# Performance work log

Hardware: AMD Instinct MI355X
Metric: run time of the kernel (lower is better)

Reference implementation:

```python
import jax, jax.numpy as jnp
import numpy as np

B, C, H, W = 4, 256, 64, 64
EPS = 1e-5

def conv1x1(x, w, b):
    # x: [B,Cin,H,W], w: [Cout,Cin], b: [Cout]
    return jnp.einsum('bchw,oc->bohw', x, w) + b[None, :, None, None]

def setup_inputs() -> dict:
    key = jax.random.key(0)
    ks = jax.random.split(key, 16)
    s = 1.0 / np.sqrt(C)
    d = {
        'x1': jax.random.normal(ks[0], (B, C, H, W), jnp.float32),
        'x2': jax.random.normal(ks[1], (B, C, H, W), jnp.float32),
        'q_w': jax.random.normal(ks[2], (C, C), jnp.float32) * s,
        'q_b': jnp.zeros((C,), jnp.float32),
        'k_w': jax.random.normal(ks[3], (C, C), jnp.float32) * s,
        'k_b': jnp.zeros((C,), jnp.float32),
        'v_w': jax.random.normal(ks[4], (C, C), jnp.float32) * s,
        'v_b': jnp.zeros((C,), jnp.float32),
        'proj_w': jax.random.normal(ks[5], (C, C), jnp.float32) * s,
        'proj_b': jnp.zeros((C,), jnp.float32),
        'bn_gamma': jnp.ones((C,), jnp.float32),
        'bn_beta': jnp.zeros((C,), jnp.float32),
        'bn_mean': jax.random.normal(ks[6], (C,), jnp.float32) * 0.1,
        'bn_var': jax.random.uniform(ks[7], (C,), jnp.float32, 0.5, 1.5),
        'gate_w': jax.random.normal(ks[8], (1, 2 * C), jnp.float32) * (1.0 / np.sqrt(2 * C)),
        'gate_b': jnp.zeros((1,), jnp.float32),
    }
    return d

def reference(x1, x2, q_w, q_b, k_w, k_b, v_w, v_b, proj_w, proj_b,
              bn_gamma, bn_beta, bn_mean, bn_var, gate_w, gate_b):
    b, c, h, w = x1.shape
    n = h * w
    scale = c ** (-0.5)
    q = conv1x1(x1, q_w, q_b).reshape(b, c, n)   # [B,C,N]
    k = conv1x1(x2, k_w, k_b).reshape(b, c, n)
    v = conv1x1(x2, v_w, v_b).reshape(b, c, n)
    attn = jnp.einsum('bcn,bcm->bnm', q, k) * scale      # [B,N,N]
    attn = jax.nn.softmax(attn, axis=-1)
    fusion = jnp.einsum('bcm,bnm->bcn', v, attn)          # v @ attn^T
    fusion = fusion.reshape(b, c, h, w)
    # proj: conv1x1 -> BN (eval, running stats) -> ReLU
    fusion = conv1x1(fusion, proj_w, proj_b)
    fusion = (fusion - bn_mean[None, :, None, None]) * (
        bn_gamma[None, :, None, None] * jax.lax.rsqrt(bn_var + EPS)[None, :, None, None]
    ) + bn_beta[None, :, None, None]
    fusion = jax.nn.relu(fusion)
    gate = jax.nn.sigmoid(conv1x1(jnp.concatenate([x1, x2], axis=1), gate_w, gate_b))  # [B,1,H,W]
    return x1 + gate * fusion
```

## Files before the change

### kernel.cpp

```cpp
#include <hip/hip_runtime.h>
#include <hip/hip_bf16.h>
#include <hip/hip_fp8.h>

#define NB   4
#define C    256
#define NPIX 4096
#define EPSV 1e-5f
#define K2   0.09016844f
#define MFIX 24.0f
#define KVB  32
#define NSPLIT 4
#define NKVS (NPIX / NSPLIT)
#define NSTEPS (NKVS / KVB)

typedef __bf16 bf16x8 __attribute__((ext_vector_type(8)));
typedef float  f32x4  __attribute__((ext_vector_type(4)));
typedef float  f32x16 __attribute__((ext_vector_type(16)));
typedef unsigned int u32x4 __attribute__((ext_vector_type(4)));
typedef __hip_bfloat16 bf16;

__device__ __forceinline__ void gload16(const void* g, void* l) {
    __builtin_amdgcn_global_load_lds(
        (const __attribute__((address_space(1))) void*)g,
        (__attribute__((address_space(3))) void*)l, 16, 0, 0);
}

__device__ __forceinline__ unsigned char to_fp8(float x) {
    return __hip_fp8_e4m3(x).__x;
}

__global__ __launch_bounds__(256) void k_transpose(
    const float* __restrict__ x1, const float* __restrict__ x2,
    const float* __restrict__ gate_w,
    const float* __restrict__ qw, const float* __restrict__ kw,
    const float* __restrict__ vw, const float* __restrict__ pw,
    bf16* __restrict__ xt1, bf16* __restrict__ xt2,
    float* __restrict__ gate_ws, bf16* __restrict__ wb)
{
    __shared__ float tile[64][65];
    const int t = threadIdx.x;
    const int z = blockIdx.z;

    if (z == 8) {
        const int sub = blockIdx.x * 4 + blockIdx.y;
        const int i0 = sub * 1024 + t * 4;
        bf16 t4[4];
#pragma unroll
        for (int j = 0; j < 4; ++j) {
            const int i = i0 + j;
            const int p = i >> 16, rem = i & 65535;
            const int o = rem >> 8, cp = rem & 255;
            const int c = cp ^ ((o & 7) << 3);
            const float* w = (p == 0) ? qw : (p == 1) ? kw : (p == 2) ? vw : pw;
            t4[j] = __float2bfloat16(w[o * 256 + c]);
        }
        *reinterpret_cast<uint64_t*>(wb + i0) = *reinterpret_cast<uint64_t*>(t4);
        return;
    }

    const int nt = blockIdx.x, ct = blockIdx.y;
    const int b = z >> 1, which = z & 1;
    const float* x = which ? x2 : x1;
    bf16* xt = which ? xt2 : xt1;
    const int n0 = nt * 64, c0 = ct * 64;

    const float* xp = x + ((size_t)b * C + c0) * NPIX + n0;
#pragma unroll
    for (int i = 0; i < 16; ++i) {
        int cl = (t >> 6) + i * 4, nl = t & 63;
        tile[cl][nl] = xp[(size_t)cl * NPIX + nl];
    }
    __syncthreads();

    {
        int nl = t & 63, qq = t >> 6;
        float s = 0.f;
#pragma unroll
        for (int i = 0; i < 16; ++i) {
            int cl = qq * 16 + i;
            s += tile[cl][nl] * gate_w[which * C + c0 + cl];
        }
        atomicAdd(&gate_ws[b * NPIX + n0 + nl], s);
    }

    bf16* xtp = xt + ((size_t)b * NPIX + n0) * C + c0;
#pragma unroll
    for (int i = 0; i < 16; ++i) {
        int nl = (t >> 6) + i * 4, cl = t & 63;
        xtp[(size_t)nl * C + cl] = __float2bfloat16(tile[cl][nl]);
    }
}

__global__ __launch_bounds__(256) void k_qkv(
    const bf16* __restrict__ xt1, const bf16* __restrict__ xt2,
    const bf16* __restrict__ wb,
    const float* __restrict__ qb, const float* __restrict__ kb,
    const float* __restrict__ vb,
    unsigned char* __restrict__ Qt, unsigned char* __restrict__ Kt,
    bf16* __restrict__ Vv)
{
    __shared__ __align__(16) char wl[32768];
    const int nblk = blockIdx.x, ot = blockIdx.y, zp = blockIdx.z;
    const int b = zp / 3, pidx = zp % 3;
    const bf16* xt = (pidx == 0) ? xt1 : xt2;
    const float* bias = (pidx == 0) ? qb : (pidx == 1) ? kb : vb;
    const int o0 = ot * 64;
    const int t = threadIdx.x;
    const int wave = t >> 6, lane = t & 63;
    const int g = lane >> 4, l15 = lane & 15;

    {
        const char* src = (const char*)(wb + ((size_t)pidx * C + o0) * C);
#pragma unroll
        for (int i = 0; i < 8; ++i) {
            const int L = i * 4096 + t * 16;
            gload16(src + L, wl + L);
        }
    }
    asm volatile("s_waitcnt vmcnt(0)" ::: "memory");
    __syncthreads();

    bf16x8 a[4][8];
#pragma unroll
    for (int ns = 0; ns < 4; ++ns) {
        const bf16* xrow = xt + ((size_t)b * NPIX + nblk * 256 + wave * 64 + ns * 16 + l15) * C;
#pragma unroll
        for (int cb = 0; cb < 8; ++cb)
            a[ns][cb] = *reinterpret_cast<const bf16x8*>(xrow + cb * 32 + 8 * g);
    }

#pragma unroll
    for (int os = 0; os < 4; ++os) {
        const int oo = o0 + os * 16;
        bf16x8 wf[8];
#pragma unroll
        for (int cb = 0; cb < 8; ++cb)
            wf[cb] = *reinterpret_cast<const bf16x8*>(
                wl + (os * 16 + l15) * 512 + ((cb * 64 + 16 * g) ^ ((l15 & 7) << 4)));

        f32x4 acc[4] = {{0,0,0,0},{0,0,0,0},{0,0,0,0},{0,0,0,0}};
#pragma unroll
        for (int cb = 0; cb < 8; ++cb) {
#pragma unroll
            for (int ns = 0; ns < 4; ++ns) {
                if (pidx < 2)
                    acc[ns] = __builtin_amdgcn_mfma_f32_16x16x32_bf16(a[ns][cb], wf[cb], acc[ns], 0, 0, 0);
                else
                    acc[ns] = __builtin_amdgcn_mfma_f32_16x16x32_bf16(wf[cb], a[ns][cb], acc[ns], 0, 0, 0);
            }
        }

        if (pidx < 2) {
            const float bv = bias[oo + l15];
            const float scl = (pidx == 0) ? K2 : 1.0f;
            unsigned char* Qk = (pidx == 0) ? Qt : Kt;
#pragma unroll
            for (int ns = 0; ns < 4; ++ns) {
                const int n0 = nblk * 256 + wave * 64 + ns * 16;
                unsigned char* dst = Qk + ((size_t)b * NPIX + n0 + 4 * g) * C + oo + l15;
#pragma unroll
                for (int r = 0; r < 4; ++r)
                    dst[(size_t)r * C] = to_fp8((acc[ns][r] + bv) * scl);
            }
        } else {
#pragma unroll
            for (int ns = 0; ns < 4; ++ns) {
                const int n0 = nblk * 256 + wave * 64 + ns * 16;
                bf16* dst = Vv + ((size_t)b * C + oo + 4 * g) * NPIX + n0 + l15;
#pragma unroll
                for (int r = 0; r < 4; ++r)
                    dst[(size_t)r * NPIX] = __float2bfloat16(acc[ns][r] + bias[oo + 4 * g + r]);
            }
        }
    }
}

#define SMEM_ATTN 49152
#define SZP ((size_t)NPIX * C)

__global__ __launch_bounds__(256, 2) void k_attn(
    const unsigned char* __restrict__ Qt, const unsigned char* __restrict__ Kt,
    const bf16* __restrict__ Vv, bf16* __restrict__ O0,
    bf16* __restrict__ O1, float2* __restrict__ mlws)
{
    extern __shared__ __align__(16) char smem[];
    const int id = blockIdx.x;
    const int combo = id & 15, nt = id >> 4;
    const int b = combo >> 2, split = combo & 3;
    const int m_base = split * NKVS;
    const int tid = threadIdx.x;
    const int wave = tid >> 6, lane = tid & 63;
    const int dl = lane & 31, hi = lane >> 5;
    const int n0 = nt * 128 + wave * 32;

    const unsigned char* Kg = Kt + (size_t)b * NPIX * C;
    const bf16* Vg = Vv + (size_t)b * C * NPIX;

    int o_k[2], o_v[4];
#pragma unroll
    for (int p = 0; p < 2; ++p) {
        const int L = p * 4096 + tid * 16;
        const int kv = L >> 8;
        const int col = (L & 255) ^ ((kv & 15) << 4);
        o_k[p] = kv * C + col;
    }
#pragma unroll
    for (int p = 0; p < 4; ++p) {
        const int L = p * 4096 + tid * 16;
        const int R = L >> 7, colx2 = L & 127;
        const int col2 = colx2 ^ (((L >> 8) & 7) << 4);
        const int d = 2 * R + (col2 >> 6);
        o_v[p] = d * NPIX + ((col2 & 63) >> 1);
    }

    long q[16];
    const unsigned char* qrow = Qt + ((size_t)b * NPIX + n0 + dl) * C + 8 * hi;
#pragma unroll
    for (int cs = 0; cs < 16; ++cs)
        q[cs] = *reinterpret_cast<const long*>(qrow + cs * 16);

    const int kRow = dl * 256, kmask = (dl & 15) << 4;
    const int vRow = (dl >> 1) * 128;
    const int vc0  = (((dl & 1) << 6) | (16 * hi)) ^ (((dl >> 2) & 7) << 4);

    f32x16 o[8];
#pragma unroll
    for (int i = 0; i < 8; ++i)
#pragma unroll
        for (int j = 0; j < 16; ++j) o[i][j] = 0.f;
    float l_run = 0.f;

    auto stage = [&](int buf, int m0) {
        char* kd = smem + buf * 24576;
        char* vd = kd + 8192;
#pragma unroll
        for (int p = 0; p < 2; ++p)
            gload16(Kg + (size_t)m0 * C + o_k[p], kd + p * 4096 + tid * 16);
#pragma unroll
        for (int p = 0; p < 4; ++p)
            gload16(Vg + o_v[p] + m0, vd + p * 4096 + tid * 16);
    };

    stage(0, m_base);
    asm volatile("s_waitcnt vmcnt(0)" ::: "memory");
    __syncthreads();

    for (int t = 0; t < NSTEPS; ++t) {
        const int buf = t & 1;
        if (t + 1 < NSTEPS) stage(buf ^ 1, m_base + (t + 1) * KVB);

        const char* Kl = smem + buf * 24576;
        const char* Vl = Kl + 8192;

        f32x16 s;
#pragma unroll
        for (int j = 0; j < 16; ++j) s[j] = 0.f;
        __builtin_amdgcn_s_setprio(1);
#pragma unroll
        for (int cs = 0; cs < 16; ++cs) {
            long kf = *reinterpret_cast<const long*>(
                Kl + kRow + ((cs * 16 + 8 * hi) ^ kmask));
            s = __builtin_amdgcn_mfma_f32_32x32x16_fp8_fp8(kf, q[cs], s, 0, 0, 0);
        }
        __builtin_amdgcn_s_setprio(0);

        float psum = 0.f;
#pragma unroll
        for (int j = 0; j < 16; ++j) {
            s[j] = exp2f(s[j] - MFIX);
            psum += s[j];
        }
        psum += __shfl_xor(psum, 32);
        l_run += psum;

        unsigned w[8];
#pragma unroll
        for (int i = 0; i < 8; ++i) {
            asm("v_cvt_pk_bf16_f32 %0, %1, %2"
                : "=v"(w[i]) : "v"(s[2 * i]), "v"(s[2 * i + 1]));
        }
        asm("v_permlane32_swap_b32 %0, %1" : "+v"(w[0]), "+v"(w[2]));
        asm("v_permlane32_swap_b32 %0, %1" : "+v"(w[1]), "+v"(w[3]));
        asm("v_permlane32_swap_b32 %0, %1" : "+v"(w[4]), "+v"(w[6]));
        asm("v_permlane32_swap_b32 %0, %1" : "+v"(w[5]), "+v"(w[7]));
        const bf16x8 pb0 = __builtin_bit_cast(bf16x8, (u32x4){w[0], w[1], w[2], w[3]});
        const bf16x8 pb1 = __builtin_bit_cast(bf16x8, (u32x4){w[4], w[5], w[6], w[7]});

        __builtin_amdgcn_s_setprio(1);
#pragma unroll
        for (int dt = 0; dt < 8; ++dt) {
            bf16x8 vf0 = *reinterpret_cast<const bf16x8*>(Vl + dt * 2048 + vRow + vc0);
            o[dt] = __builtin_amdgcn_mfma_f32_32x32x16_bf16(vf0, pb0, o[dt], 0, 0, 0);
            bf16x8 vf1 = *reinterpret_cast<const bf16x8*>(Vl + dt * 2048 + vRow + (vc0 ^ 32));
            o[dt] = __builtin_amdgcn_mfma_f32_32x32x16_bf16(vf1, pb1, o[dt], 0, 0, 0);
        }
        __builtin_amdgcn_s_setprio(0);

        asm volatile("s_waitcnt vmcnt(0)" ::: "memory");
        __syncthreads();
    }

    const int pp = split * NB + b;
    bf16* base = (pp < 8) ? (O0 + (size_t)pp * SZP) : (O1 + (size_t)(pp - 8) * SZP);
    const float invl = 1.0f / l_run;
    bf16* orow = base + (size_t)(n0 + dl) * C;
#pragma unroll
    for (int dt = 0; dt < 8; ++dt) {
#pragma unroll
        for (int a = 0; a < 4; ++a) {
            bf16 t4[4];
#pragma unroll
            for (int r = 0; r < 4; ++r)
                t4[r] = __float2bfloat16(o[dt][4 * a + r] * invl);
            *reinterpret_cast<uint64_t*>(orow + dt * 32 + 8 * a + 4 * hi) =
                *reinterpret_cast<uint64_t*>(t4);
        }
    }
    if (lane < 32)
        mlws[(size_t)pp * NPIX + n0 + dl] = make_float2(MFIX, l_run);
}

__global__ __launch_bounds__(256) void k_combine(
    const bf16* __restrict__ O0, const bf16* __restrict__ O1,
    const float2* __restrict__ ml, bf16* __restrict__ Ot)
{
    const int tid = blockIdx.x * 256 + threadIdx.x;
    const int c8 = tid & 31;
    const int rest = tid >> 5;
    const int n = rest & 4095;
    const int b = rest >> 12;

    float2 a[NSPLIT];
#pragma unroll
    for (int s = 0; s < NSPLIT; ++s)
        a[s] = ml[(size_t)(s * NB + b) * NPIX + n];
    float M = fmaxf(fmaxf(a[0].x, a[1].x), fmaxf(a[2].x, a[3].x));
    float w[NSPLIT], tot = 0.f;
#pragma unroll
    for (int s = 0; s < NSPLIT; ++s) { w[s] = exp2f(a[s].x - M) * a[s].y; tot += w[s]; }
    float rs = 1.0f / tot;
#pragma unroll
    for (int s = 0; s < NSPLIT; ++s) w[s] *= rs;

    const size_t off = (size_t)n * C + c8 * 8;
    float acc[8] = {0,0,0,0,0,0,0,0};
#pragma unroll
    for (int s = 0; s < NSPLIT; ++s) {
        const int pp = s * NB + b;
        const bf16* src = ((pp < 8) ? (O0 + (size_t)pp * SZP)
                                    : (O1 + (size_t)(pp - 8) * SZP)) + off;
        bf16x8 x = *reinterpret_cast<const bf16x8*>(src);
#pragma unroll
        for (int j = 0; j < 8; ++j) acc[j] += w[s] * (float)x[j];
    }
    bf16 outv[8];
#pragma unroll
    for (int j = 0; j < 8; ++j) outv[j] = __float2bfloat16(acc[j]);
    *reinterpret_cast<bf16x8*>(Ot + ((size_t)b * NPIX + n) * C + c8 * 8) =
        *reinterpret_cast<bf16x8*>(outv);
}

__global__ __launch_bounds__(256) void k_proj(
    const bf16* __restrict__ Ot, const bf16* __restrict__ wb,
    const float* __restrict__ pb, const float* __restrict__ bn_g,
    const float* __restrict__ bn_b, const float* __restrict__ bn_m,
    const float* __restrict__ bn_v, const float* __restrict__ gate_ws,
    const float* __restrict__ gate_b, const float* __restrict__ x1,
    float* __restrict__ out)
{
    __shared__ __align__(16) char wl[32768];
    const int nblk = blockIdx.x, ot = blockIdx.y, b = blockIdx.z;
    const int o0 = ot * 64;
    const int t = threadIdx.x;
    const int wave = t >> 6, lane = t & 63;
    const int g = lane >> 4, l15 = lane & 15;

    {
        const char* src = (const char*)(wb + ((size_t)3 * C + o0) * C);
#pragma unroll
        for (int i = 0; i < 8; ++i) {
            const int L = i * 4096 + t * 16;
            gload16(src + L, wl + L);
        }
    }
    asm volatile("s_waitcnt vmcnt(0)" ::: "memory");
    __syncthreads();

    bf16x8 bfr[2][8];
#pragma unroll
    for (int ns = 0; ns < 2; ++ns) {
        const bf16* orow = Ot + ((size_t)b * NPIX + nblk * 128 + wave * 32 + ns * 16 + l15) * C;
#pragma unroll
        for (int cb = 0; cb < 8; ++cb)
            bfr[ns][cb] = *reinterpret_cast<const bf16x8*>(orow + cb * 32 + 8 * g);
    }
    const float gb = gate_b[0];

#pragma unroll
    for (int os = 0; os < 4; ++os) {
        const int oo = o0 + os * 16;
        bf16x8 wf[8];
#pragma unroll
        for (int cb = 0; cb < 8; ++cb)
            wf[cb] = *reinterpret_cast<const bf16x8*>(
                wl + (os * 16 + l15) * 512 + ((cb * 64 + 16 * g) ^ ((l15 & 7) << 4)));

        f32x4 acc[2] = {{0,0,0,0},{0,0,0,0}};
#pragma unroll
        for (int cb = 0; cb < 8; ++cb) {
            acc[0] = __builtin_amdgcn_mfma_f32_16x16x32_bf16(wf[cb], bfr[0][cb], acc[0], 0, 0, 0);
            acc[1] = __builtin_amdgcn_mfma_f32_16x16x32_bf16(wf[cb], bfr[1][cb], acc[1], 0, 0, 0);
        }

#pragma unroll
        for (int ns = 0; ns < 2; ++ns) {
            const int n0 = nblk * 128 + wave * 32 + ns * 16;
            float gsum = gate_ws[b * NPIX + n0 + l15];
            float gate = 1.f / (1.f + __expf(-(gsum + gb)));
#pragma unroll
            for (int r = 0; r < 4; ++r) {
                int oc = oo + 4 * g + r;
                float scl = bn_g[oc] * rsqrtf(bn_v[oc] + EPSV);
                float v = (acc[ns][r] + pb[oc] - bn_m[oc]) * scl + bn_b[oc];
                v = fmaxf(v, 0.f);
                size_t idx = ((size_t)b * C + oc) * NPIX + n0 + l15;
                out[idx] = x1[idx] + gate * v;
            }
        }
    }
}

extern "C" void kernel_launch(void* const* d_in, const int* in_sizes, int n_in,
                              void* d_out, int out_size, void* d_ws, size_t ws_size,
                              hipStream_t stream)
{
    const float* x1  = (const float*)d_in[0];
    const float* x2  = (const float*)d_in[1];
    const float* q_w = (const float*)d_in[2];
    const float* q_b = (const float*)d_in[3];
    const float* k_w = (const float*)d_in[4];
    const float* k_b = (const float*)d_in[5];
    const float* v_w = (const float*)d_in[6];
    const float* v_b = (const float*)d_in[7];
    const float* p_w = (const float*)d_in[8];
    const float* p_b = (const float*)d_in[9];
    const float* bn_g = (const float*)d_in[10];
    const float* bn_b = (const float*)d_in[11];
    const float* bn_m = (const float*)d_in[12];
    const float* bn_v = (const float*)d_in[13];
    const float* g_w  = (const float*)d_in[14];
    const float* g_b  = (const float*)d_in[15];
    float* out = (float*)d_out;

    const size_t szBF = (size_t)NB * NPIX * C * sizeof(bf16);
    char* p = (char*)d_ws;
    bf16* xt1 = (bf16*)p; p += szBF;
    bf16* xt2 = (bf16*)p; p += szBF;
    char* QtS = p; p += szBF;
    char* KtS = p; p += szBF;
    bf16* Vv  = (bf16*)p; p += szBF;
    float* gate_ws = (float*)p; p += (size_t)NB * NPIX * sizeof(float);
    float2* mlws = (float2*)p; p += (size_t)16 * NPIX * sizeof(float2);
    bf16* wb = (bf16*)p;

    unsigned char* Qt8 = (unsigned char*)QtS;
    unsigned char* Kt8 = (unsigned char*)KtS;

    bf16* O0 = (bf16*)d_out;
    bf16* O1 = xt1;
    bf16* Ot = (bf16*)QtS;

    hipFuncSetAttribute((const void*)k_attn,
                        hipFuncAttributeMaxDynamicSharedMemorySize, SMEM_ATTN);

    hipMemsetAsync(gate_ws, 0, (size_t)NB * NPIX * sizeof(float), stream);
    k_transpose<<<dim3(64, 4, 9),  256, 0, stream>>>(x1, x2, g_w, q_w, k_w, v_w, p_w,
                                                     xt1, xt2, gate_ws, wb);
    k_qkv     <<<dim3(16, 4, 12), 256, 0, stream>>>(xt1, xt2, wb, q_b, k_b, v_b,
                                                    Qt8, Kt8, Vv);
    k_attn    <<<dim3(512), 256, SMEM_ATTN, stream>>>(Qt8, Kt8, Vv, O0, O1, mlws);
    k_combine <<<dim3(2048), 256, 0, stream>>>(O0, O1, mlws, Ot);
    k_proj    <<<dim3(32, 4, 4),  256, 0, stream>>>(Ot, wb, p_b, bn_g, bn_b, bn_m,
                                                    bn_v, gate_ws, g_b, x1, out);
}
```

Before: 141.9 us.

## Switch attention kernel to 16x16 MFMA tiles with LDS-staged P and more blocks

```diff
diff --git a/kernel.cpp b/kernel.cpp
--- a/kernel.cpp
+++ b/kernel.cpp
@@ -15,7 +15,6 @@
 
 typedef __bf16 bf16x8 __attribute__((ext_vector_type(8)));
 typedef float  f32x4  __attribute__((ext_vector_type(4)));
-typedef float  f32x16 __attribute__((ext_vector_type(16)));
 typedef unsigned int u32x4 __attribute__((ext_vector_type(4)));
 typedef __hip_bfloat16 bf16;
 
@@ -175,10 +174,10 @@
     }
 }
 
-#define SMEM_ATTN 49152
+#define SMEM_ATTN 54272
 #define SZP ((size_t)NPIX * C)
 
-__global__ __launch_bounds__(256, 2) void k_attn(
+__global__ __launch_bounds__(256, 3) void k_attn(
     const unsigned char* __restrict__ Qt, const unsigned char* __restrict__ Kt,
     const bf16* __restrict__ Vv, bf16* __restrict__ O0,
     bf16* __restrict__ O1, float2* __restrict__ mlws)
@@ -190,8 +189,8 @@
     const int m_base = split * NKVS;
     const int tid = threadIdx.x;
     const int wave = tid >> 6, lane = tid & 63;
-    const int dl = lane & 31, hi = lane >> 5;
-    const int n0 = nt * 128 + wave * 32;
+    const int l15 = lane & 15, g4 = lane >> 4;
+    const int n0 = nt * 64 + wave * 16;
 
     const unsigned char* Kg = Kt + (size_t)b * NPIX * C;
     const bf16* Vg = Vv + (size_t)b * C * NPIX;
@@ -213,21 +212,20 @@
         o_v[p] = d * NPIX + ((col2 & 63) >> 1);
     }
 
-    long q[16];
-    const unsigned char* qrow = Qt + ((size_t)b * NPIX + n0 + dl) * C + 8 * hi;
-#pragma unroll
-    for (int cs = 0; cs < 16; ++cs)
-        q[cs] = *reinterpret_cast<const long*>(qrow + cs * 16);
-
-    const int kRow = dl * 256, kmask = (dl & 15) << 4;
-    const int vRow = (dl >> 1) * 128;
-    const int vc0  = (((dl & 1) << 6) | (16 * hi)) ^ (((dl >> 2) & 7) << 4);
-
-    f32x16 o[8];
-#pragma unroll
-    for (int i = 0; i < 8; ++i)
-#pragma unroll
-        for (int j = 0; j < 16; ++j) o[i][j] = 0.f;
+    long q[8];
+    const unsigned char* qrow = Qt + ((size_t)b * NPIX + n0 + l15) * C + 8 * g4;
+#pragma unroll
+    for (int cs = 0; cs < 8; ++cs)
+        q[cs] = *reinterpret_cast<const long*>(qrow + cs * 32);
+
+    char* Pl = smem + 49152 + wave * 1280;
+    const int kRow = l15 * 256, kmask = l15 << 4;
+    const int vR = (l15 >> 1) * 128;
+    const int vc = ((((l15 & 1) << 6) | (16 * g4)) ^ ((l15 >> 2) << 4));
+
+    f32x4 o[16];
+#pragma unroll
+    for (int i = 0; i < 16; ++i) o[i] = {0.f, 0.f, 0.f, 0.f};
     float l_run = 0.f;
 
     auto stage = [&](int buf, int m0) {
@@ -252,47 +250,48 @@
         const char* Kl = smem + buf * 24576;
         const char* Vl = Kl + 8192;
 
-        f32x16 s;
-#pragma unroll
-        for (int j = 0; j < 16; ++j) s[j] = 0.f;
+        f32x4 s0 = {0,0,0,0}, s1 = {0,0,0,0};
         __builtin_amdgcn_s_setprio(1);
 #pragma unroll
-        for (int cs = 0; cs < 16; ++cs) {
+        for (int cs = 0; cs < 8; ++cs) {
             long kf = *reinterpret_cast<const long*>(
-                Kl + kRow + ((cs * 16 + 8 * hi) ^ kmask));
-            s = __builtin_amdgcn_mfma_f32_32x32x16_fp8_fp8(kf, q[cs], s, 0, 0, 0);
+                Kl + kRow + ((cs * 32 + 8 * g4) ^ kmask));
+            s0 = __builtin_amdgcn_mfma_f32_16x16x32_fp8_fp8(kf, q[cs], s0, 0, 0, 0);
+        }
+#pragma unroll
+        for (int cs = 0; cs < 8; ++cs) {
+            long kf = *reinterpret_cast<const long*>(
+                Kl + 4096 + kRow + ((cs * 32 + 8 * g4) ^ kmask));
+            s1 = __builtin_amdgcn_mfma_f32_16x16x32_fp8_fp8(kf, q[cs], s1, 0, 0, 0);
         }
         __builtin_amdgcn_s_setprio(0);
 
         float psum = 0.f;
 #pragma unroll
-        for (int j = 0; j < 16; ++j) {
-            s[j] = exp2f(s[j] - MFIX);
-            psum += s[j];
-        }
+        for (int r = 0; r < 4; ++r) { s0[r] = exp2f(s0[r] - MFIX); psum += s0[r]; }
+#pragma unroll
+        for (int r = 0; r < 4; ++r) { s1[r] = exp2f(s1[r] - MFIX); psum += s1[r]; }
+        psum += __shfl_xor(psum, 16);
         psum += __shfl_xor(psum, 32);
         l_run += psum;
 
-        unsigned w[8];
-#pragma unroll
-        for (int i = 0; i < 8; ++i) {
-            asm("v_cvt_pk_bf16_f32 %0, %1, %2"
-                : "=v"(w[i]) : "v"(s[2 * i]), "v"(s[2 * i + 1]));
-        }
-        asm("v_permlane32_swap_b32 %0, %1" : "+v"(w[0]), "+v"(w[2]));
-        asm("v_permlane32_swap_b32 %0, %1" : "+v"(w[1]), "+v"(w[3]));
-        asm("v_permlane32_swap_b32 %0, %1" : "+v"(w[4]), "+v"(w[6]));
-        asm("v_permlane32_swap_b32 %0, %1" : "+v"(w[5]), "+v"(w[7]));
-        const bf16x8 pb0 = __builtin_bit_cast(bf16x8, (u32x4){w[0], w[1], w[2], w[3]});
-        const bf16x8 pb1 = __builtin_bit_cast(bf16x8, (u32x4){w[4], w[5], w[6], w[7]});
+        unsigned w0, w1, w2, w3;
+        asm("v_cvt_pk_bf16_f32 %0, %1, %2" : "=v"(w0) : "v"(s0[0]), "v"(s0[1]));
+        asm("v_cvt_pk_bf16_f32 %0, %1, %2" : "=v"(w1) : "v"(s0[2]), "v"(s0[3]));
+        asm("v_cvt_pk_bf16_f32 %0, %1, %2" : "=v"(w2) : "v"(s1[0]), "v"(s1[1]));
+        asm("v_cvt_pk_bf16_f32 %0, %1, %2" : "=v"(w3) : "v"(s1[2]), "v"(s1[3]));
+        *reinterpret_cast<uint64_t*>(Pl + l15 * 80 + 8 * g4) =
+            (uint64_t)w0 | ((uint64_t)w1 << 32);
+        *reinterpret_cast<uint64_t*>(Pl + l15 * 80 + 32 + 8 * g4) =
+            (uint64_t)w2 | ((uint64_t)w3 << 32);
+        const bf16x8 pf = *reinterpret_cast<const bf16x8*>(Pl + l15 * 80 + 16 * g4);
 
         __builtin_amdgcn_s_setprio(1);
 #pragma unroll
-        for (int dt = 0; dt < 8; ++dt) {
-            bf16x8 vf0 = *reinterpret_cast<const bf16x8*>(Vl + dt * 2048 + vRow + vc0);
-            o[dt] = __builtin_amdgcn_mfma_f32_32x32x16_bf16(vf0, pb0, o[dt], 0, 0, 0);
-            bf16x8 vf1 = *reinterpret_cast<const bf16x8*>(Vl + dt * 2048 + vRow + (vc0 ^ 32));
-            o[dt] = __builtin_amdgcn_mfma_f32_32x32x16_bf16(vf1, pb1, o[dt], 0, 0, 0);
+        for (int dt = 0; dt < 16; ++dt) {
+            bf16x8 vf = *reinterpret_cast<const bf16x8*>(
+                Vl + dt * 1024 + vR + (vc ^ ((dt & 1) << 6)));
+            o[dt] = __builtin_amdgcn_mfma_f32_16x16x32_bf16(vf, pf, o[dt], 0, 0, 0);
         }
         __builtin_amdgcn_s_setprio(0);
 
@@ -303,21 +302,18 @@
     const int pp = split * NB + b;
     bf16* base = (pp < 8) ? (O0 + (size_t)pp * SZP) : (O1 + (size_t)(pp - 8) * SZP);
     const float invl = 1.0f / l_run;
-    bf16* orow = base + (size_t)(n0 + dl) * C;
-#pragma unroll
-    for (int dt = 0; dt < 8; ++dt) {
-#pragma unroll
-        for (int a = 0; a < 4; ++a) {
-            bf16 t4[4];
-#pragma unroll
-            for (int r = 0; r < 4; ++r)
-                t4[r] = __float2bfloat16(o[dt][4 * a + r] * invl);
-            *reinterpret_cast<uint64_t*>(orow + dt * 32 + 8 * a + 4 * hi) =
-                *reinterpret_cast<uint64_t*>(t4);
-        }
-    }
-    if (lane < 32)
-        mlws[(size_t)pp * NPIX + n0 + dl] = make_float2(MFIX, l_run);
+    bf16* orow = base + (size_t)(n0 + l15) * C;
+#pragma unroll
+    for (int dt = 0; dt < 16; ++dt) {
+        bf16 t4[4];
+#pragma unroll
+        for (int r = 0; r < 4; ++r)
+            t4[r] = __float2bfloat16(o[dt][r] * invl);
+        *reinterpret_cast<uint64_t*>(orow + dt * 16 + 4 * g4) =
+            *reinterpret_cast<uint64_t*>(t4);
+    }
+    if (lane < 16)
+        mlws[(size_t)pp * NPIX + n0 + l15] = make_float2(MFIX, l_run);
 }
 
 __global__ __launch_bounds__(256) void k_combine(
@@ -478,7 +474,7 @@
                                                      xt1, xt2, gate_ws, wb);
     k_qkv     <<<dim3(16, 4, 12), 256, 0, stream>>>(xt1, xt2, wb, q_b, k_b, v_b,
                                                     Qt8, Kt8, Vv);
-    k_attn    <<<dim3(512), 256, SMEM_ATTN, stream>>>(Qt8, Kt8, Vv, O0, O1, mlws);
+    k_attn    <<<dim3(1024), 256, SMEM_ATTN, stream>>>(Qt8, Kt8, Vv, O0, O1, mlws);
     k_combine <<<dim3(2048), 256, 0, stream>>>(O0, O1, mlws, Ot);
     k_proj    <<<dim3(32, 4, 4),  256, 0, stream>>>(Ot, wb, p_b, bn_g, bn_b, bn_m,
                                                     bn_v, gate_ws, g_b, x1, out);
```

Result: slower. 171.5 us (+20.9%).
